# Optimization experiments

Measured on AMD Instinct MI355X. Metric: run time of the kernel, lower is better.

## Reference

```python
import jax, jax.numpy as jnp
import numpy as np

N_NODES = 100000
N_EDGES = 1600000
D = 128
N_LAYERS = 3
BN_EPS = 1e-5
NORM_EPS = 1e-12


def setup_inputs() -> dict:
    key = jax.random.key(0)
    ks = jax.random.split(key, 4)
    x = jax.random.normal(ks[0], (N_NODES, D), dtype=jnp.float32)
    edge_index = jax.random.randint(ks[1], (2, N_EDGES), 0, N_NODES, dtype=jnp.int32)
    W1 = jax.random.normal(ks[2], (N_LAYERS, D, D), dtype=jnp.float32) * (1.0 / np.sqrt(D))
    W2 = jax.random.normal(ks[3], (N_LAYERS, D, D), dtype=jnp.float32) * (1.0 / np.sqrt(D))
    return {
        "x": x,
        "edge_index": edge_index,
        "W1": W1,
        "b1": jnp.zeros((N_LAYERS, D), jnp.float32),
        "g1": jnp.ones((N_LAYERS, D), jnp.float32),
        "be1": jnp.zeros((N_LAYERS, D), jnp.float32),
        "W2": W2,
        "b2": jnp.zeros((N_LAYERS, D), jnp.float32),
        "g_out": jnp.ones((N_LAYERS - 1, D), jnp.float32),
        "b_out": jnp.zeros((N_LAYERS - 1, D), jnp.float32),
    }


def _batchnorm(h, gamma, beta):
    # BatchNorm1d in training mode: biased batch statistics over nodes.
    mu = jnp.mean(h, axis=0)
    var = jnp.var(h, axis=0)
    return (h - mu) * jax.lax.rsqrt(var + BN_EPS) * gamma + beta


def reference(x, edge_index, W1, b1, g1, be1, W2, b2, g_out, b_out):
    src, dst = edge_index[0], edge_index[1]
    h = x
    for i in range(N_LAYERS):
        # GINConv, eps=0: (1+eps)*x + sum of neighbor messages (scatter-add)
        agg = jax.ops.segment_sum(h[src], dst, num_segments=N_NODES)
        h = h + agg
        # inner MLP: Linear -> BN -> ReLU -> Linear
        h = h @ W1[i] + b1[i]
        h = jax.nn.relu(_batchnorm(h, g1[i], be1[i]))
        h = h @ W2[i] + b2[i]
        if i < N_LAYERS - 1:
            h = jax.nn.relu(_batchnorm(h, g_out[i], b_out[i]))
    # F.normalize(p=2, dim=-1) clamps the norm at 1e-12
    norm = jnp.linalg.norm(h, axis=-1, keepdims=True)
    return h / jnp.maximum(norm, NORM_EPS)
```

## Files before the change

kernel.cpp:

```cpp
#include <hip/hip_runtime.h>

#define M_NODES 100000
#define PADM 100032
#define DIM 128
#define N_EDGES_TOT 1600000
#define NBKT 256
#define NPB 391
#define BKT_CAP 8192
#define INVN 1e-5f

typedef unsigned int uint;
typedef unsigned short ushort;
typedef __attribute__((ext_vector_type(8))) short bf16x8;
typedef __attribute__((ext_vector_type(4))) float f32x4;

__device__ __forceinline__ float bflo(uint u) { return __uint_as_float(u << 16); }
__device__ __forceinline__ float bfhi(uint u) { return __uint_as_float(u & 0xffff0000u); }
__device__ __forceinline__ float bf2f(ushort h) { return __uint_as_float(((uint)h) << 16); }
__device__ __forceinline__ ushort f2bf(float f) {
    uint u = __float_as_uint(f);
    return (ushort)((u + 0x7fffu + ((u >> 16) & 1u)) >> 16);
}

__global__ void k_zerof(float* p, int n) {
    int i = blockIdx.x * 256 + threadIdx.x;
    if (i < n) p[i] = 0.f;
}

__global__ void k_cvt(const float* __restrict__ x, ushort* __restrict__ xb,
                      int n4) {
    int i = blockIdx.x * 256 + threadIdx.x;
    if (i >= n4) return;
    float4 v = ((const float4*)x)[i];
    uint2 r;
    r.x = (uint)f2bf(v.x) | ((uint)f2bf(v.y) << 16);
    r.y = (uint)f2bf(v.z) | ((uint)f2bf(v.w) << 16);
    ((uint2*)xb)[i] = r;
}

__global__ void k_wprep(const float* __restrict__ W1,
                        const float* __restrict__ W2, ushort* __restrict__ Wh,
                        ushort* __restrict__ Wl) {
    int i = blockIdx.x * 256 + threadIdx.x;
    if (i >= 6 * 16384) return;
    int l = i >> 14;
    int r = i & 16383;
    int n = r >> 7, k = r & 127;
    const float* W = (l < 3) ? (W1 + l * 16384) : (W2 + (l - 3) * 16384);
    float w = W[k * 128 + n];
    ushort h = f2bf(w);
    Wh[i] = h;
    Wl[i] = f2bf(w - bf2f(h));
}

__global__ void k_bhist(const int* __restrict__ dst, int* __restrict__ cntM,
                        int nE, int nChunks) {
    __shared__ int h[NBKT];
    const int chunk = blockIdx.x, t = threadIdx.x;
    h[t] = 0;
    __syncthreads();
    const int e0 = chunk * 2048;
#pragma unroll
    for (int k = 0; k < 8; ++k) {
        int e = e0 + k * 256 + t;
        if (e < nE) atomicAdd(&h[dst[e] / NPB], 1);
    }
    __syncthreads();
    cntM[t * nChunks + chunk] = h[t];
}

__global__ void k_scanA(int* __restrict__ cnt, int* __restrict__ bsum, int n) {
    __shared__ int s[256];
    int t = threadIdx.x, i = blockIdx.x * 256 + t;
    int v = (i < n) ? cnt[i] : 0;
    s[t] = v;
    __syncthreads();
#pragma unroll
    for (int o = 1; o < 256; o <<= 1) {
        int a = (t >= o) ? s[t - o] : 0;
        __syncthreads();
        s[t] += a;
        __syncthreads();
    }
    if (i < n) cnt[i] = s[t] - v;
    if (t == 255) bsum[blockIdx.x] = s[255];
}

__global__ void k_scanB(int* bsum, int nB) {
    __shared__ int s[1024];
    int t = threadIdx.x;
    int v = (t < nB) ? bsum[t] : 0;
    s[t] = v;
    __syncthreads();
#pragma unroll
    for (int o = 1; o < 1024; o <<= 1) {
        int a = (t >= o) ? s[t - o] : 0;
        __syncthreads();
        s[t] += a;
        __syncthreads();
    }
    if (t < nB) bsum[t] = s[t] - v;
}

__global__ void k_scanC(int* __restrict__ excl, const int* __restrict__ bsum) {
    int i = blockIdx.x * 256 + threadIdx.x;
    excl[i] += bsum[blockIdx.x];
}

__global__ void k_pairs(const int* __restrict__ src, const int* __restrict__ dst,
                        const int* __restrict__ exclM, int2* __restrict__ pairs,
                        int nE, int nChunks) {
    __shared__ int base[NBKT];
    const int chunk = blockIdx.x, t = threadIdx.x;
    base[t] = exclM[t * nChunks + chunk];
    __syncthreads();
    const int e0 = chunk * 2048;
#pragma unroll
    for (int k = 0; k < 8; ++k) {
        int e = e0 + k * 256 + t;
        if (e < nE) {
            int d = dst[e];
            int pos = atomicAdd(&base[d / NPB], 1);
            pairs[pos] = make_int2(d, src[e]);
        }
    }
}

__global__ void k_csrD(const int2* __restrict__ pairs,
                       const int* __restrict__ exclM, int nChunks,
                       int* __restrict__ rowptr, int* __restrict__ srcs,
                       int nE) {
    __shared__ int cnt[512];
    __shared__ int scn[512];
    __shared__ int sl[BKT_CAP];
    const int b = blockIdx.x, t = threadIdx.x;
    const int base = exclM[b * nChunks];
    const int next = (b == NBKT - 1) ? nE : exclM[(b + 1) * nChunks];
    const int count = next - base;
    const int nodeBase = b * NPB;
    const int nNodes = min(NPB, M_NODES - nodeBase);
    cnt[t] = 0;
    cnt[t + 256] = 0;
    __syncthreads();
    for (int i = t; i < count; i += 256)
        atomicAdd(&cnt[pairs[base + i].x - nodeBase], 1);
    __syncthreads();
    scn[t] = cnt[t];
    scn[t + 256] = cnt[t + 256];
    __syncthreads();
#pragma unroll
    for (int o = 1; o < 512; o <<= 1) {
        int a0 = (t >= o) ? scn[t - o] : 0;
        int a1 = scn[t + 256 - o];
        __syncthreads();
        scn[t] += a0;
        scn[t + 256] += a1;
        __syncthreads();
    }
    int o0 = scn[t] - cnt[t];
    int o1 = scn[t + 256] - cnt[t + 256];
    __syncthreads();
    cnt[t] = o0;
    cnt[t + 256] = o1;
    if (t < nNodes) rowptr[nodeBase + t] = base + o0;
    if (t + 256 < nNodes) rowptr[nodeBase + t + 256] = base + o1;
    if (b == 0 && t == 0) rowptr[M_NODES] = nE;
    __syncthreads();
    const bool inLds = (count <= BKT_CAP);
    for (int i = t; i < count; i += 256) {
        int2 p = pairs[base + i];
        int pos = atomicAdd(&cnt[p.x - nodeBase], 1);
        if (inLds) sl[pos] = p.y;
        else srcs[base + pos] = p.y;
    }
    __syncthreads();
    if (inLds)
        for (int i = t; i < count; i += 256) srcs[base + i] = sl[i];
}

__global__ void k_gather(const ushort* __restrict__ h,
                         const int* __restrict__ rowptr,
                         const int* __restrict__ srcs,
                         const float* __restrict__ bnstats,
                         const float* __restrict__ gamma,
                         const float* __restrict__ beta,
                         ushort* __restrict__ AGh, ushort* __restrict__ AGl,
                         int M) {
    int t = threadIdx.x;
    int node = blockIdx.x * 8 + (t >> 5);
    if (node >= M) return;
    int c = (t & 31) * 4;
    const bool bn = (bnstats != nullptr);
    float4 sc = make_float4(1.f, 1.f, 1.f, 1.f);
    float4 sh = make_float4(0.f, 0.f, 0.f, 0.f);
    if (bn) {
        float4 sum4 = *(const float4*)(bnstats + c);
        float4 sq4 = *(const float4*)(bnstats + 128 + c);
        float4 g4 = *(const float4*)(gamma + c);
        float4 b4 = *(const float4*)(beta + c);
        float mu, var, s;
        mu = sum4.x * INVN; var = sq4.x * INVN - mu * mu;
        s = g4.x * rsqrtf(var + 1e-5f); sc.x = s; sh.x = b4.x - mu * s;
        mu = sum4.y * INVN; var = sq4.y * INVN - mu * mu;
        s = g4.y * rsqrtf(var + 1e-5f); sc.y = s; sh.y = b4.y - mu * s;
        mu = sum4.z * INVN; var = sq4.z * INVN - mu * mu;
        s = g4.z * rsqrtf(var + 1e-5f); sc.z = s; sh.z = b4.z - mu * s;
        mu = sum4.w * INVN; var = sq4.w * INVN - mu * mu;
        s = g4.w * rsqrtf(var + 1e-5f); sc.w = s; sh.w = b4.w - mu * s;
    }
    int beg = rowptr[node];
    int end = rowptr[node + 1];

    uint2 v = *(const uint2*)(h + (size_t)node * DIM + c);
    float a0 = bflo(v.x), a1 = bfhi(v.x), a2 = bflo(v.y), a3 = bfhi(v.y);
    if (bn) {
        a0 = fmaxf(fmaf(a0, sc.x, sh.x), 0.f);
        a1 = fmaxf(fmaf(a1, sc.y, sh.y), 0.f);
        a2 = fmaxf(fmaf(a2, sc.z, sh.z), 0.f);
        a3 = fmaxf(fmaf(a3, sc.w, sh.w), 0.f);
    }
    float b0 = 0.f, b1 = 0.f, b2 = 0.f, b3 = 0.f;

    int j = beg;
    for (; j + 4 <= end; j += 4) {
        int s0 = srcs[j], s1 = srcs[j + 1], s2 = srcs[j + 2], s3 = srcs[j + 3];
        uint2 g0 = *(const uint2*)(h + (size_t)s0 * DIM + c);
        uint2 g1 = *(const uint2*)(h + (size_t)s1 * DIM + c);
        uint2 g2 = *(const uint2*)(h + (size_t)s2 * DIM + c);
        uint2 g3 = *(const uint2*)(h + (size_t)s3 * DIM + c);
        if (bn) {
            a0 += fmaxf(fmaf(bflo(g0.x), sc.x, sh.x), 0.f);
            a1 += fmaxf(fmaf(bfhi(g0.x), sc.y, sh.y), 0.f);
            a2 += fmaxf(fmaf(bflo(g0.y), sc.z, sh.z), 0.f);
            a3 += fmaxf(fmaf(bfhi(g0.y), sc.w, sh.w), 0.f);
            b0 += fmaxf(fmaf(bflo(g1.x), sc.x, sh.x), 0.f);
            b1 += fmaxf(fmaf(bfhi(g1.x), sc.y, sh.y), 0.f);
            b2 += fmaxf(fmaf(bflo(g1.y), sc.z, sh.z), 0.f);
            b3 += fmaxf(fmaf(bfhi(g1.y), sc.w, sh.w), 0.f);
            a0 += fmaxf(fmaf(bflo(g2.x), sc.x, sh.x), 0.f);
            a1 += fmaxf(fmaf(bfhi(g2.x), sc.y, sh.y), 0.f);
            a2 += fmaxf(fmaf(bflo(g2.y), sc.z, sh.z), 0.f);
            a3 += fmaxf(fmaf(bfhi(g2.y), sc.w, sh.w), 0.f);
            b0 += fmaxf(fmaf(bflo(g3.x), sc.x, sh.x), 0.f);
            b1 += fmaxf(fmaf(bfhi(g3.x), sc.y, sh.y), 0.f);
            b2 += fmaxf(fmaf(bflo(g3.y), sc.z, sh.z), 0.f);
            b3 += fmaxf(fmaf(bfhi(g3.y), sc.w, sh.w), 0.f);
        } else {
            a0 += bflo(g0.x); a1 += bfhi(g0.x); a2 += bflo(g0.y); a3 += bfhi(g0.y);
            b0 += bflo(g1.x); b1 += bfhi(g1.x); b2 += bflo(g1.y); b3 += bfhi(g1.y);
            a0 += bflo(g2.x); a1 += bfhi(g2.x); a2 += bflo(g2.y); a3 += bfhi(g2.y);
            b0 += bflo(g3.x); b1 += bfhi(g3.x); b2 += bflo(g3.y); b3 += bfhi(g3.y);
        }
    }
    for (; j < end; ++j) {
        int s = srcs[j];
        uint2 g = *(const uint2*)(h + (size_t)s * DIM + c);
        if (bn) {
            a0 += fmaxf(fmaf(bflo(g.x), sc.x, sh.x), 0.f);
            a1 += fmaxf(fmaf(bfhi(g.x), sc.y, sh.y), 0.f);
            a2 += fmaxf(fmaf(bflo(g.y), sc.z, sh.z), 0.f);
            a3 += fmaxf(fmaf(bfhi(g.y), sc.w, sh.w), 0.f);
        } else {
            a0 += bflo(g.x); a1 += bfhi(g.x); a2 += bflo(g.y); a3 += bfhi(g.y);
        }
    }
    float s0 = a0 + b0, s1 = a1 + b1, s2 = a2 + b2, s3 = a3 + b3;
    ushort h0 = f2bf(s0), h1 = f2bf(s1), h2 = f2bf(s2), h3 = f2bf(s3);
    ushort l0 = f2bf(s0 - bf2f(h0)), l1 = f2bf(s1 - bf2f(h1));
    ushort l2 = f2bf(s2 - bf2f(h2)), l3 = f2bf(s3 - bf2f(h3));
    uint2 hp, lp;
    hp.x = (uint)h0 | ((uint)h1 << 16);
    hp.y = (uint)h2 | ((uint)h3 << 16);
    lp.x = (uint)l0 | ((uint)l1 << 16);
    lp.y = (uint)l2 | ((uint)l3 << 16);
    size_t ix = (size_t)node * DIM + c;
    *(uint2*)(AGh + ix) = hp;
    *(uint2*)(AGl + ix) = lp;
}

__global__ void __launch_bounds__(256, 3) k_gemmA(
    ushort* __restrict__ Ah, ushort* __restrict__ Al,
    const ushort* __restrict__ Wh, const ushort* __restrict__ Wl,
    const float* __restrict__ bias, float* __restrict__ statSlot, int M) {
    __shared__ ushort lds[16384];
    const int t = threadIdx.x;
    const int w = t >> 6, lane = t & 63, rq = lane >> 4, rc = lane & 15;
    const int row0 = blockIdx.x * 64;

    bf16x8 wh[4][2], wl[4][2];
#pragma unroll
    for (int kc = 0; kc < 4; ++kc)
#pragma unroll
        for (int jj = 0; jj < 2; ++jj) {
            size_t off = (size_t)(w * 32 + jj * 16 + rc) * DIM + kc * 32 + rq * 8;
            wh[kc][jj] = *(const bf16x8*)(Wh + off);
            wl[kc][jj] = *(const bf16x8*)(Wl + off);
        }

#pragma unroll
    for (int i = 0; i < 8; ++i) {
        int idx = t + i * 256;
        int pl = idx >> 10;
        int r = (idx >> 4) & 63;
        int cb = idx & 15;
        const ushort* p = pl ? Al : Ah;
        uint4 v = *(const uint4*)(p + (size_t)(row0 + r) * DIM + cb * 8);
        *(uint4*)((char*)lds + pl * 16384 + r * 256 +
                  ((cb * 16) ^ ((r & 15) << 4))) = v;
    }
    __syncthreads();

    f32x4 acc[4][2];
#pragma unroll
    for (int i = 0; i < 4; ++i)
#pragma unroll
        for (int jj = 0; jj < 2; ++jj) acc[i][jj] = (f32x4){0.f, 0.f, 0.f, 0.f};

#pragma unroll
    for (int kc = 0; kc < 4; ++kc) {
        const int kb = kc * 64 + rq * 16;
#pragma unroll
        for (int i = 0; i < 4; ++i) {
            int lr = i * 16 + rc;
            int so = lr * 256 + (kb ^ ((lr & 15) << 4));
            bf16x8 ah = *(const bf16x8*)((char*)lds + so);
            bf16x8 al = *(const bf16x8*)((char*)lds + 16384 + so);
#pragma unroll
            for (int jj = 0; jj < 2; ++jj) {
                acc[i][jj] = __builtin_amdgcn_mfma_f32_16x16x32_bf16(ah, wh[kc][jj], acc[i][jj], 0, 0, 0);
                acc[i][jj] = __builtin_amdgcn_mfma_f32_16x16x32_bf16(al, wh[kc][jj], acc[i][jj], 0, 0, 0);
                acc[i][jj] = __builtin_amdgcn_mfma_f32_16x16x32_bf16(ah, wl[kc][jj], acc[i][jj], 0, 0, 0);
            }
        }
    }

    float bc[2] = {bias[w * 32 + rc], bias[w * 32 + 16 + rc]};
    float csum[2] = {0.f, 0.f}, csq[2] = {0.f, 0.f};
#pragma unroll
    for (int i = 0; i < 4; ++i)
#pragma unroll
        for (int r = 0; r < 4; ++r) {
            int row = row0 + i * 16 + rq * 4 + r;
            if (row < M) {
#pragma unroll
                for (int jj = 0; jj < 2; ++jj) {
                    float o = acc[i][jj][r] + bc[jj];
                    ushort hi = f2bf(o);
                    size_t ix = (size_t)row * DIM + w * 32 + jj * 16 + rc;
                    Ah[ix] = hi;
                    Al[ix] = f2bf(o - bf2f(hi));
                    csum[jj] += o;
                    csq[jj] += o * o;
                }
            }
        }
#pragma unroll
    for (int jj = 0; jj < 2; ++jj) {
        csum[jj] += __shfl_xor(csum[jj], 16);
        csum[jj] += __shfl_xor(csum[jj], 32);
        csq[jj] += __shfl_xor(csq[jj], 16);
        csq[jj] += __shfl_xor(csq[jj], 32);
    }
    if (lane < 16) {
        atomicAdd(statSlot + w * 32 + rc, csum[0]);
        atomicAdd(statSlot + w * 32 + 16 + rc, csum[1]);
        atomicAdd(statSlot + 128 + w * 32 + rc, csq[0]);
        atomicAdd(statSlot + 128 + w * 32 + 16 + rc, csq[1]);
    }
}

__global__ void __launch_bounds__(256, 3) k_gemmB(
    const ushort* __restrict__ Ah, const ushort* __restrict__ Al,
    const ushort* __restrict__ Wh, const ushort* __restrict__ Wl,
    const float* __restrict__ bias, const float* __restrict__ bnstats,
    const float* __restrict__ gamma, const float* __restrict__ beta,
    ushort* __restrict__ Cb, float* __restrict__ outF,
    float* __restrict__ statSlot, int M) {
    __shared__ ushort lds[16384];
    const int t = threadIdx.x;
    const int w = t >> 6, lane = t & 63, rq = lane >> 4, rc = lane & 15;
    const int row0 = blockIdx.x * 64;

    bf16x8 wh[4][2], wl[4][2];
#pragma unroll
    for (int kc = 0; kc < 4; ++kc)
#pragma unroll
        for (int jj = 0; jj < 2; ++jj) {
            size_t off = (size_t)(w * 32 + jj * 16 + rc) * DIM + kc * 32 + rq * 8;
            wh[kc][jj] = *(const bf16x8*)(Wh + off);
            wl[kc][jj] = *(const bf16x8*)(Wl + off);
        }

    const int cb = t & 15;
    float sc8[8], sh8[8];
#pragma unroll
    for (int e = 0; e < 8; ++e) {
        int ch = cb * 8 + e;
        float mu = bnstats[ch] * INVN;
        float var = bnstats[128 + ch] * INVN - mu * mu;
        float s = gamma[ch] * rsqrtf(var + 1e-5f);
        sc8[e] = s;
        sh8[e] = beta[ch] - mu * s;
    }

#pragma unroll
    for (int i = 0; i < 4; ++i) {
        int idx = t + i * 256;
        int r = idx >> 4;
        size_t gix = (size_t)(row0 + r) * DIM + cb * 8;
        uint4 H = *(const uint4*)(Ah + gix);
        uint4 L = *(const uint4*)(Al + gix);
        uint hu[4] = {H.x, H.y, H.z, H.w};
        uint lu[4] = {L.x, L.y, L.z, L.w};
        uint oh[4], ol[4];
#pragma unroll
        for (int e = 0; e < 4; ++e) {
            float v0 = bflo(hu[e]) + bflo(lu[e]);
            float v1 = bfhi(hu[e]) + bfhi(lu[e]);
            v0 = fmaxf(fmaf(v0, sc8[2 * e], sh8[2 * e]), 0.f);
            v1 = fmaxf(fmaf(v1, sc8[2 * e + 1], sh8[2 * e + 1]), 0.f);
            ushort h0 = f2bf(v0), h1 = f2bf(v1);
            oh[e] = (uint)h0 | ((uint)h1 << 16);
            ol[e] = (uint)f2bf(v0 - bf2f(h0)) | ((uint)f2bf(v1 - bf2f(h1)) << 16);
        }
        char* dst = (char*)lds + r * 256 + ((cb * 16) ^ ((r & 15) << 4));
        *(uint4*)dst = make_uint4(oh[0], oh[1], oh[2], oh[3]);
        *(uint4*)(dst + 16384) = make_uint4(ol[0], ol[1], ol[2], ol[3]);
    }
    __syncthreads();

    f32x4 acc[4][2];
#pragma unroll
    for (int i = 0; i < 4; ++i)
#pragma unroll
        for (int jj = 0; jj < 2; ++jj) acc[i][jj] = (f32x4){0.f, 0.f, 0.f, 0.f};

#pragma unroll
    for (int kc = 0; kc < 4; ++kc) {
        const int kb = kc * 64 + rq * 16;
#pragma unroll
        for (int i = 0; i < 4; ++i) {
            int lr = i * 16 + rc;
            int so = lr * 256 + (kb ^ ((lr & 15) << 4));
            bf16x8 ah = *(const bf16x8*)((char*)lds + so);
            bf16x8 al = *(const bf16x8*)((char*)lds + 16384 + so);
#pragma unroll
            for (int jj = 0; jj < 2; ++jj) {
                acc[i][jj] = __builtin_amdgcn_mfma_f32_16x16x32_bf16(ah, wh[kc][jj], acc[i][jj], 0, 0, 0);
                acc[i][jj] = __builtin_amdgcn_mfma_f32_16x16x32_bf16(al, wh[kc][jj], acc[i][jj], 0, 0, 0);
                acc[i][jj] = __builtin_amdgcn_mfma_f32_16x16x32_bf16(ah, wl[kc][jj], acc[i][jj], 0, 0, 0);
            }
        }
    }

    float bc[2] = {bias[w * 32 + rc], bias[w * 32 + 16 + rc]};

    if (outF) {
#pragma unroll
        for (int i = 0; i < 4; ++i)
#pragma unroll
            for (int r = 0; r < 4; ++r)
#pragma unroll
                for (int jj = 0; jj < 2; ++jj) acc[i][jj][r] += bc[jj];
        __syncthreads();
        float* nr = (float*)lds;
#pragma unroll
        for (int i = 0; i < 4; ++i)
#pragma unroll
            for (int r = 0; r < 4; ++r) {
                float ss = acc[i][0][r] * acc[i][0][r] + acc[i][1][r] * acc[i][1][r];
                ss += __shfl_xor(ss, 1);
                ss += __shfl_xor(ss, 2);
                ss += __shfl_xor(ss, 4);
                ss += __shfl_xor(ss, 8);
                if (rc == 0) nr[(i * 16 + rq * 4 + r) * 4 + w] = ss;
            }
        __syncthreads();
#pragma unroll
        for (int i = 0; i < 4; ++i)
#pragma unroll
            for (int r = 0; r < 4; ++r) {
                int lrow = i * 16 + rq * 4 + r;
                float4 q = *(const float4*)(nr + lrow * 4);
                float inv = 1.f / fmaxf(sqrtf(q.x + q.y + q.z + q.w), 1e-12f);
                int row = row0 + lrow;
                if (row < M) {
                    outF[(size_t)row * DIM + w * 32 + rc] = acc[i][0][r] * inv;
                    outF[(size_t)row * DIM + w * 32 + 16 + rc] = acc[i][1][r] * inv;
                }
            }
        return;
    }

    float csum[2] = {0.f, 0.f}, csq[2] = {0.f, 0.f};
#pragma unroll
    for (int i = 0; i < 4; ++i)
#pragma unroll
        for (int r = 0; r < 4; ++r) {
            int row = row0 + i * 16 + rq * 4 + r;
            if (row < M) {
#pragma unroll
                for (int jj = 0; jj < 2; ++jj) {
                    float o = acc[i][jj][r] + bc[jj];
                    Cb[(size_t)row * DIM + w * 32 + jj * 16 + rc] = f2bf(o);
                    csum[jj] += o;
                    csq[jj] += o * o;
                }
            }
        }
#pragma unroll
    for (int jj = 0; jj < 2; ++jj) {
        csum[jj] += __shfl_xor(csum[jj], 16);
        csum[jj] += __shfl_xor(csum[jj], 32);
        csq[jj] += __shfl_xor(csq[jj], 16);
        csq[jj] += __shfl_xor(csq[jj], 32);
    }
    if (lane < 16) {
        atomicAdd(statSlot + w * 32 + rc, csum[0]);
        atomicAdd(statSlot + w * 32 + 16 + rc, csum[1]);
        atomicAdd(statSlot + 128 + w * 32 + rc, csq[0]);
        atomicAdd(statSlot + 128 + w * 32 + 16 + rc, csq[1]);
    }
}

extern "C" void kernel_launch(void* const* d_in, const int* in_sizes, int n_in,
                              void* d_out, int out_size, void* d_ws,
                              size_t ws_size, hipStream_t stream) {
    const float* x = (const float*)d_in[0];
    const int* ei = (const int*)d_in[1];
    const float* W1 = (const float*)d_in[2];
    const float* b1 = (const float*)d_in[3];
    const float* g1 = (const float*)d_in[4];
    const float* be1 = (const float*)d_in[5];
    const float* W2 = (const float*)d_in[6];
    const float* b2 = (const float*)d_in[7];
    const float* g_out = (const float*)d_in[8];
    const float* b_out = (const float*)d_in[9];
    float* out = (float*)d_out;

    const int M = M_NODES;
    const int E = N_EDGES_TOT;
    const size_t NM = (size_t)M * DIM;
    const size_t PM = (size_t)PADM * DIM;
    const int nChunks = (E + 2047) / 2048;
    const int nMat = NBKT * nChunks;

    ushort* AGh = (ushort*)d_ws;
    ushort* AGl = AGh + PM;
    ushort* B0 = AGl + PM;
    ushort* Wh = B0 + NM;
    ushort* Wl = Wh + 6 * 16384;
    float* st = (float*)(Wl + 6 * 16384);
    float* stA0 = st;
    float* stA1 = st + 256;
    float* stA2 = st + 512;
    float* stB0 = st + 768;
    float* stB1 = st + 1024;
    int2* pairs = (int2*)(st + 1280);
    int* rowptr = (int*)(pairs + E);
    int* cntM = rowptr + (M + 2);
    int* bsum = cntM + nMat;
    int* srcs = bsum + 1024;

    const int* src = ei;
    const int* dst = ei + E;

    const int gemmGrid = PADM / 64;
    const int gathGrid = (M + 7) / 8;

    k_bhist<<<nChunks, 256, 0, stream>>>(dst, cntM, E, nChunks);
    k_scanA<<<nMat / 256, 256, 0, stream>>>(cntM, bsum, nMat);
    k_scanB<<<1, 1024, 0, stream>>>(bsum, nMat / 256);
    k_scanC<<<nMat / 256, 256, 0, stream>>>(cntM, bsum);
    k_pairs<<<nChunks, 256, 0, stream>>>(src, dst, cntM, pairs, E, nChunks);
    k_csrD<<<NBKT, 256, 0, stream>>>(pairs, cntM, nChunks, rowptr, srcs, E);

    k_cvt<<<(int)((NM / 4 + 255) / 256), 256, 0, stream>>>(x, B0, (int)(NM / 4));
    k_wprep<<<(6 * 16384 + 255) / 256, 256, 0, stream>>>(W1, W2, Wh, Wl);
    k_zerof<<<5, 256, 0, stream>>>(st, 1280);

    k_gather<<<gathGrid, 256, 0, stream>>>(B0, rowptr, srcs, nullptr, nullptr,
                                           nullptr, AGh, AGl, M);
    k_gemmA<<<gemmGrid, 256, 0, stream>>>(AGh, AGl, Wh, Wl, b1, stA0, M);
    k_gemmB<<<gemmGrid, 256, 0, stream>>>(AGh, AGl, Wh + 3 * 16384, Wl + 3 * 16384,
                                          b2, stA0, g1, be1, B0, nullptr, stB0, M);

    k_gather<<<gathGrid, 256, 0, stream>>>(B0, rowptr, srcs, stB0, g_out, b_out,
                                           AGh, AGl, M);
    k_gemmA<<<gemmGrid, 256, 0, stream>>>(AGh, AGl, Wh + 16384, Wl + 16384,
                                          b1 + 128, stA1, M);
    k_gemmB<<<gemmGrid, 256, 0, stream>>>(AGh, AGl, Wh + 4 * 16384, Wl + 4 * 16384,
                                          b2 + 128, stA1, g1 + 128, be1 + 128,
                                          B0, nullptr, stB1, M);

    k_gather<<<gathGrid, 256, 0, stream>>>(B0, rowptr, srcs, stB1, g_out + 128,
                                           b_out + 128, AGh, AGl, M);
    k_gemmA<<<gemmGrid, 256, 0, stream>>>(AGh, AGl, Wh + 2 * 16384, Wl + 2 * 16384,
                                          b1 + 256, stA2, M);
    k_gemmB<<<gemmGrid, 256, 0, stream>>>(AGh, AGl, Wh + 5 * 16384, Wl + 5 * 16384,
                                          b2 + 256, stA2, g1 + 256, be1 + 256,
                                          nullptr, out, nullptr, M);
}
```

Measured before the change: 569.4 us.

## Store GEMM-A output in MFMA fragment order and stage GEMM-B output through LDS

GEMM-A now stages its hi/lo bf16 output through LDS and writes it to global memory pre-swizzled in the MFMA A-fragment order. GEMM-B can then load its A operands directly into registers with coalesced 16-byte loads and apply the BN+ReLU on the fly, skipping the LDS staging and its barrier. BN coefficients are computed once per block into LDS instead of per thread, and the GEMM-B bf16 output is also staged through LDS so global stores are full 16-byte rows. The intermediate buffer layout changes, so it is only valid if no other consumer reads Ah/Al in row-major form. The padded tail rows are written unconditionally, which relies on PADM allocation.

```diff
diff --git a/kernel.cpp b/kernel.cpp
--- a/kernel.cpp
+++ b/kernel.cpp
@@ -336,24 +336,42 @@
 
     float bc[2] = {bias[w * 32 + rc], bias[w * 32 + 16 + rc]};
     float csum[2] = {0.f, 0.f}, csq[2] = {0.f, 0.f};
+
+    __syncthreads();
 #pragma unroll
     for (int i = 0; i < 4; ++i)
 #pragma unroll
         for (int r = 0; r < 4; ++r) {
-            int row = row0 + i * 16 + rq * 4 + r;
-            if (row < M) {
-#pragma unroll
-                for (int jj = 0; jj < 2; ++jj) {
-                    float o = acc[i][jj][r] + bc[jj];
-                    ushort hi = f2bf(o);
-                    size_t ix = (size_t)row * DIM + w * 32 + jj * 16 + rc;
-                    Ah[ix] = hi;
-                    Al[ix] = f2bf(o - bf2f(hi));
-                    csum[jj] += o;
-                    csq[jj] += o * o;
-                }
+            int lrow = i * 16 + rq * 4 + r;
+            bool live = (row0 + lrow) < M;
+#pragma unroll
+            for (int jj = 0; jj < 2; ++jj) {
+                float o = acc[i][jj][r] + bc[jj];
+                ushort hi = f2bf(o);
+                ushort lo = f2bf(o - bf2f(hi));
+                int off = lrow * 256 +
+                          (((w * 32 + jj * 16 + rc) * 2) ^ ((lrow & 15) << 4));
+                *(ushort*)((char*)lds + off) = hi;
+                *(ushort*)((char*)lds + 16384 + off) = lo;
+                if (live) { csum[jj] += o; csq[jj] += o * o; }
             }
         }
+    __syncthreads();
+    {
+        int lrow = w * 16 + (lane & 15);
+        int kq = lane >> 4;
+        ushort* dH = Ah + (size_t)row0 * DIM;
+        ushort* dL = Al + (size_t)row0 * DIM;
+#pragma unroll
+        for (int kc = 0; kc < 4; ++kc) {
+            int off = lrow * 256 + ((kc * 64 + kq * 16) ^ ((lrow & 15) << 4));
+            uint4 H = *(uint4*)((char*)lds + off);
+            uint4 L = *(uint4*)((char*)lds + 16384 + off);
+            size_t go = ((size_t)(w * 4 + kc) * 64 + lane) * 8;
+            *(uint4*)(dH + go) = H;
+            *(uint4*)(dL + go) = L;
+        }
+    }
 #pragma unroll
     for (int jj = 0; jj < 2; ++jj) {
         csum[jj] += __shfl_xor(csum[jj], 16);
@@ -376,7 +394,7 @@
     const float* __restrict__ gamma, const float* __restrict__ beta,
     ushort* __restrict__ Cb, float* __restrict__ outF,
     float* __restrict__ statSlot, int M) {
-    __shared__ ushort lds[16384];
+    __shared__ char smem[16384];
     const int t = threadIdx.x;
     const int w = t >> 6, lane = t & 63, rq = lane >> 4, rc = lane & 15;
     const int row0 = blockIdx.x * 64;
@@ -391,43 +409,19 @@
             wl[kc][jj] = *(const bf16x8*)(Wl + off);
         }
 
-    const int cb = t & 15;
-    float sc8[8], sh8[8];
-#pragma unroll
-    for (int e = 0; e < 8; ++e) {
-        int ch = cb * 8 + e;
-        float mu = bnstats[ch] * INVN;
-        float var = bnstats[128 + ch] * INVN - mu * mu;
-        float s = gamma[ch] * rsqrtf(var + 1e-5f);
-        sc8[e] = s;
-        sh8[e] = beta[ch] - mu * s;
-    }
-
-#pragma unroll
-    for (int i = 0; i < 4; ++i) {
-        int idx = t + i * 256;
-        int r = idx >> 4;
-        size_t gix = (size_t)(row0 + r) * DIM + cb * 8;
-        uint4 H = *(const uint4*)(Ah + gix);
-        uint4 L = *(const uint4*)(Al + gix);
-        uint hu[4] = {H.x, H.y, H.z, H.w};
-        uint lu[4] = {L.x, L.y, L.z, L.w};
-        uint oh[4], ol[4];
-#pragma unroll
-        for (int e = 0; e < 4; ++e) {
-            float v0 = bflo(hu[e]) + bflo(lu[e]);
-            float v1 = bfhi(hu[e]) + bfhi(lu[e]);
-            v0 = fmaxf(fmaf(v0, sc8[2 * e], sh8[2 * e]), 0.f);
-            v1 = fmaxf(fmaf(v1, sc8[2 * e + 1], sh8[2 * e + 1]), 0.f);
-            ushort h0 = f2bf(v0), h1 = f2bf(v1);
-            oh[e] = (uint)h0 | ((uint)h1 << 16);
-            ol[e] = (uint)f2bf(v0 - bf2f(h0)) | ((uint)f2bf(v1 - bf2f(h1)) << 16);
-        }
-        char* dst = (char*)lds + r * 256 + ((cb * 16) ^ ((r & 15) << 4));
-        *(uint4*)dst = make_uint4(oh[0], oh[1], oh[2], oh[3]);
-        *(uint4*)(dst + 16384) = make_uint4(ol[0], ol[1], ol[2], ol[3]);
-    }
-    __syncthreads();
+    float* coef = (float*)smem;
+    if (t < 128) {
+        float mu = bnstats[t] * INVN;
+        float var = bnstats[128 + t] * INVN - mu * mu;
+        float s = gamma[t] * rsqrtf(var + 1e-5f);
+        coef[t] = s;
+        coef[128 + t] = beta[t] - mu * s;
+    }
+    __syncthreads();
+
+    const ushort* pH = Ah + (size_t)row0 * DIM;
+    const ushort* pL = Al + (size_t)row0 * DIM;
+    const int kq8 = (lane >> 4) * 8;
 
     f32x4 acc[4][2];
 #pragma unroll
@@ -437,13 +431,35 @@
 
 #pragma unroll
     for (int kc = 0; kc < 4; ++kc) {
-        const int kb = kc * 64 + rq * 16;
+        float sc8[8], sh8[8];
+#pragma unroll
+        for (int e = 0; e < 8; ++e) {
+            sc8[e] = coef[kc * 32 + kq8 + e];
+            sh8[e] = coef[128 + kc * 32 + kq8 + e];
+        }
 #pragma unroll
         for (int i = 0; i < 4; ++i) {
-            int lr = i * 16 + rc;
-            int so = lr * 256 + (kb ^ ((lr & 15) << 4));
-            bf16x8 ah = *(const bf16x8*)((char*)lds + so);
-            bf16x8 al = *(const bf16x8*)((char*)lds + 16384 + so);
+            size_t go = ((size_t)(i * 4 + kc) * 64 + lane) * 8;
+            uint4 H = *(const uint4*)(pH + go);
+            uint4 L = *(const uint4*)(pL + go);
+            uint hu[4] = {H.x, H.y, H.z, H.w};
+            uint lu[4] = {L.x, L.y, L.z, L.w};
+            uint oh[4], ol[4];
+#pragma unroll
+            for (int e = 0; e < 4; ++e) {
+                float v0 = bflo(hu[e]) + bflo(lu[e]);
+                float v1 = bfhi(hu[e]) + bfhi(lu[e]);
+                v0 = fmaxf(fmaf(v0, sc8[2 * e], sh8[2 * e]), 0.f);
+                v1 = fmaxf(fmaf(v1, sc8[2 * e + 1], sh8[2 * e + 1]), 0.f);
+                ushort h0 = f2bf(v0), h1 = f2bf(v1);
+                oh[e] = (uint)h0 | ((uint)h1 << 16);
+                ol[e] = (uint)f2bf(v0 - bf2f(h0)) |
+                        ((uint)f2bf(v1 - bf2f(h1)) << 16);
+            }
+            uint4 AH = make_uint4(oh[0], oh[1], oh[2], oh[3]);
+            uint4 AL = make_uint4(ol[0], ol[1], ol[2], ol[3]);
+            bf16x8 ah = *(bf16x8*)&AH;
+            bf16x8 al = *(bf16x8*)&AL;
 #pragma unroll
             for (int jj = 0; jj < 2; ++jj) {
                 acc[i][jj] = __builtin_amdgcn_mfma_f32_16x16x32_bf16(ah, wh[kc][jj], acc[i][jj], 0, 0, 0);
@@ -463,7 +479,7 @@
 #pragma unroll
                 for (int jj = 0; jj < 2; ++jj) acc[i][jj][r] += bc[jj];
         __syncthreads();
-        float* nr = (float*)lds;
+        float* nr = (float*)smem;
 #pragma unroll
         for (int i = 0; i < 4; ++i)
 #pragma unroll
@@ -493,21 +509,33 @@
     }
 
     float csum[2] = {0.f, 0.f}, csq[2] = {0.f, 0.f};
+    __syncthreads();
 #pragma unroll
     for (int i = 0; i < 4; ++i)
 #pragma unroll
         for (int r = 0; r < 4; ++r) {
-            int row = row0 + i * 16 + rq * 4 + r;
-            if (row < M) {
-#pragma unroll
-                for (int jj = 0; jj < 2; ++jj) {
-                    float o = acc[i][jj][r] + bc[jj];
-                    Cb[(size_t)row * DIM + w * 32 + jj * 16 + rc] = f2bf(o);
-                    csum[jj] += o;
-                    csq[jj] += o * o;
-                }
+            int lrow = i * 16 + rq * 4 + r;
+            bool live = (row0 + lrow) < M;
+#pragma unroll
+            for (int jj = 0; jj < 2; ++jj) {
+                float o = acc[i][jj][r] + bc[jj];
+                int off = lrow * 256 +
+                          (((w * 32 + jj * 16 + rc) * 2) ^ ((lrow & 15) << 4));
+                *(ushort*)(smem + off) = f2bf(o);
+                if (live) { csum[jj] += o; csq[jj] += o * o; }
             }
         }
+    __syncthreads();
+#pragma unroll
+    for (int it = 0; it < 4; ++it) {
+        int idx = t + it * 256;
+        int row = idx >> 4, cb = idx & 15;
+        int grow = row0 + row;
+        if (grow < M) {
+            uint4 v = *(uint4*)(smem + row * 256 + ((cb * 16) ^ ((row & 15) << 4)));
+            *(uint4*)(Cb + (size_t)grow * DIM + cb * 8) = v;
+        }
+    }
 #pragma unroll
     for (int jj = 0; jj < 2; ++jj) {
         csum[jj] += __shfl_xor(csum[jj], 16);
```

After: 576.5 us. Within noise of the previous version (+1.3%).
